# Kernel tuning notes

Measured on AMD Instinct MI355X. Metric: run time of the kernel, lower is better.

## Reference

```python
import jax, jax.numpy as jnp
import numpy as np
from jax import lax

REGION_SIZE = 5      # local window side (init kwarg)
BANDWIDTH = 0.1      # KDE kernel bandwidth (init kwarg)
NUM_BINS = 256       # intensity histogram bins
EPS = 1e-10


def setup_inputs() -> dict:
    key = jax.random.key(0)
    # image-like inputs in [0, 255] to match the 256 intensity bins
    x = jax.random.uniform(key, (8, 3, 96, 96), dtype=jnp.float32) * 255.0
    return {"x": x}


def reference(x):
    # x: [B, C, H, W]
    bins = jnp.arange(NUM_BINS, dtype=x.dtype)            # [256]
    # derivative-of-sigmoid KDE kernel evaluated at each (pixel, bin) pair
    d = (x[..., None] - bins) / BANDWIDTH                 # [B,C,H,W,256]
    sig = jax.nn.sigmoid(d)
    k = sig * (1.0 - sig)                                 # [B,C,H,W,256]
    # accumulate kernel mass over the region_size x region_size window
    # (stride 1, centered -> SAME padding), per bin
    p = lax.reduce_window(
        k, jnp.float32(0.0), lax.add,
        window_dimensions=(1, 1, REGION_SIZE, REGION_SIZE, 1),
        window_strides=(1, 1, 1, 1, 1),
        padding='SAME')                                   # [B,C,H,W,256]
    # normalize to a probability distribution over bins
    p = p / (jnp.sum(p, axis=-1, keepdims=True) + EPS)
    # Shannon entropy per pixel
    return -jnp.sum(p * jnp.log(p + EPS), axis=-1)        # [B,C,H,W]
```

## Files before the change

### kernel.cpp

```cpp
#include <hip/hip_runtime.h>
#include <hip/hip_fp16.h>
#include <stdint.h>


#define W   96
#define H   96
#define WP  100
#define IMG (W*H)
#define IMGP (WP*WP)
#define TPB 256

#if __has_builtin(__builtin_amdgcn_logf)
__device__ __forceinline__ float rawlog2(float v) {
    return __builtin_amdgcn_logf(v);
}
#else
__device__ __forceinline__ float rawlog2(float v) {
    float r;
    asm("v_log_f32 %0, %1\n\ts_nop 1" : "=v"(r) : "v"(v));
    return r;
}
#endif

__global__ __launch_bounds__(TPB) void mass_kernel(
    const float* __restrict__ x, uint4* __restrict__ wm, int total2)
{
    const int pid = blockIdx.x * TPB + threadIdx.x;
    if (pid >= total2) return;
    const int x2  = pid % WP;
    const int y2  = (pid / WP) % WP;
    const int img = pid / IMGP;

    uint4 e;
    if (x2 >= 2 && x2 < WP - 2 && y2 >= 2 && y2 < WP - 2) {
        const float v  = x[img * IMG + (y2 - 2) * W + (x2 - 2)];
        const int   b0 = (int)v;
        const float f  = v - (float)b0;
        const float E  = __expf(-10.f * f);
        const float E2 = __expf(10.f * f - 10.f);
        const float r0 = __builtin_amdgcn_rcpf(1.f + E);
        const float r1 = __builtin_amdgcn_rcpf(1.f + E2);
        const float k0 = E  * r0 * r0;
        const float k1 = E2 * r1 * r1;
        const __half2 hk = __floats2half2_rn(k0, k1);
        const float2  kc = __half22float2(hk);
        e.x = __builtin_bit_cast(uint32_t, hk);
        e.y = (uint32_t)(b0 << 4);
        e.z = __builtin_bit_cast(uint32_t, kc.x);
        e.w = __builtin_bit_cast(uint32_t, kc.y);
    } else {
        e.x = 0u;
        e.y = (uint32_t)(1 << 20);
        e.z = 0u;
        e.w = 0u;
    }
    wm[pid] = e;
}

__global__ __launch_bounds__(TPB) void entropy_kde_kernel(
    const uint4* __restrict__ wm, float* __restrict__ out)
{
    const int px   = blockIdx.x * TPB + threadIdx.x;
    const int xcol = px % W;
    const int y    = (px / W) % H;
    const int img  = px / IMG;
    const uint4* __restrict__ wb = wm + img * IMGP + y * WP + xcol;

    uint64_t pk64[25];
    int      bsh [25];
    float S0 = 0.f, S1 = 0.f;
    float T0 = 0.f, T1 = 0.f, T2a = 0.f, T3 = 0.f;

    #pragma unroll
    for (int i = 0; i < 25; ++i) {
        const int dy = i / 5, dx = i % 5;
        const uint4 m = wb[dy * WP + dx];
        const int   A  = (int)m.y + 32;
        const float k0 = __builtin_bit_cast(float, m.z);
        const float k1 = __builtin_bit_cast(float, m.w);
        if (i & 1) S1 += k0 + k1; else S0 += k0 + k1;

        uint32_t Ppk = 0u;
        #pragma unroll
        for (int j = 0; j < i; ++j) {
            int s = A - bsh[j];
            s = s < 0 ? 0 : (s > 63 ? 63 : s);
            const uint32_t t = (uint32_t)(pk64[j] >> s);
            const __half2 sum = __hadd2(__builtin_bit_cast(__half2, Ppk),
                                        __builtin_bit_cast(__half2, t));
            Ppk = __builtin_bit_cast(uint32_t, sum);
        }
        const float2 P  = __half22float2(__builtin_bit_cast(__half2, Ppk));
        const float z0 = P.x + k0, z1 = P.y + k1;
        const float t4 = z0  * rawlog2(z0  + 1e-10f) - P.x * rawlog2(P.x + 1e-10f)
                       + z1  * rawlog2(z1  + 1e-10f) - P.y * rawlog2(P.y + 1e-10f);
        if      ((i & 3) == 0) T0  += t4;
        else if ((i & 3) == 1) T1  += t4;
        else if ((i & 3) == 2) T2a += t4;
        else                   T3  += t4;

        bsh[i]  = (int)m.y;
        pk64[i] = ((uint64_t)m.x) << 32;
    }

    const float S  = (S0 + S1) + 1e-10f;
    const float T  = (T0 + T1) + (T2a + T3);
    out[px] = 0.69314718056f * (rawlog2(S) - T / S);
}

extern "C" void kernel_launch(void* const* d_in, const int* in_sizes, int n_in,
                              void* d_out, int out_size, void* d_ws, size_t ws_size,
                              hipStream_t stream)
{
    const float* x = (const float*)d_in[0];
    float* out = (float*)d_out;
    uint4* wm  = (uint4*)d_ws;
    const int total  = in_sizes[0];
    const int total2 = (total / IMG) * IMGP;
    mass_kernel<<<(total2 + TPB - 1) / TPB, TPB, 0, stream>>>(x, wm, total2);
    entropy_kde_kernel<<<total / TPB, TPB, 0, stream>>>(wm, out);
}
```

Measured before the change: 70.24 us.

## Shrink intermediate record to uint2 and reorder pairwise loop to outer-source form

The per-pixel intermediate record drops from 16 to 8 bytes: the float copies of the two kernel values are removed and reconstructed from the packed half2 in the entropy kernel. The pairwise accumulation loop is restructured so each earlier window element j is broadcast-shifted into all later accumulators P[i], with all 25 loads issued up front. The aim is to halve workspace traffic and shorten the serial dependency chain per accumulator. In exchange, 25 live half2 accumulators add register pressure, and the S sums now use the half-rounded values.

```diff
diff --git a/kernel.cpp b/kernel.cpp
--- a/kernel.cpp
+++ b/kernel.cpp
@@ -23,7 +23,7 @@
 #endif
 
 __global__ __launch_bounds__(TPB) void mass_kernel(
-    const float* __restrict__ x, uint4* __restrict__ wm, int total2)
+    const float* __restrict__ x, uint2* __restrict__ wm, int total2)
 {
     const int pid = blockIdx.x * TPB + threadIdx.x;
     if (pid >= total2) return;
@@ -31,7 +31,7 @@
     const int y2  = (pid / WP) % WP;
     const int img = pid / IMGP;
 
-    uint4 e;
+    uint2 e;
     if (x2 >= 2 && x2 < WP - 2 && y2 >= 2 && y2 < WP - 2) {
         const float v  = x[img * IMG + (y2 - 2) * W + (x2 - 2)];
         const int   b0 = (int)v;
@@ -43,68 +43,69 @@
         const float k0 = E  * r0 * r0;
         const float k1 = E2 * r1 * r1;
         const __half2 hk = __floats2half2_rn(k0, k1);
-        const float2  kc = __half22float2(hk);
         e.x = __builtin_bit_cast(uint32_t, hk);
         e.y = (uint32_t)(b0 << 4);
-        e.z = __builtin_bit_cast(uint32_t, kc.x);
-        e.w = __builtin_bit_cast(uint32_t, kc.y);
     } else {
         e.x = 0u;
         e.y = (uint32_t)(1 << 20);
-        e.z = 0u;
-        e.w = 0u;
     }
     wm[pid] = e;
 }
 
 __global__ __launch_bounds__(TPB) void entropy_kde_kernel(
-    const uint4* __restrict__ wm, float* __restrict__ out)
+    const uint2* __restrict__ wm, float* __restrict__ out)
 {
     const int px   = blockIdx.x * TPB + threadIdx.x;
     const int xcol = px % W;
     const int y    = (px / W) % H;
     const int img  = px / IMG;
-    const uint4* __restrict__ wb = wm + img * IMGP + y * WP + xcol;
+    const uint2* __restrict__ wb = wm + img * IMGP + y * WP + xcol;
 
-    uint64_t pk64[25];
-    int      bsh [25];
-    float S0 = 0.f, S1 = 0.f;
-    float T0 = 0.f, T1 = 0.f, T2a = 0.f, T3 = 0.f;
+    uint32_t pk [25];
+    int      bsh[25];
+    uint32_t P  [25];
 
     #pragma unroll
     for (int i = 0; i < 25; ++i) {
-        const int dy = i / 5, dx = i % 5;
-        const uint4 m = wb[dy * WP + dx];
-        const int   A  = (int)m.y + 32;
-        const float k0 = __builtin_bit_cast(float, m.z);
-        const float k1 = __builtin_bit_cast(float, m.w);
-        if (i & 1) S1 += k0 + k1; else S0 += k0 + k1;
+        const uint2 m = wb[(i / 5) * WP + (i % 5)];
+        pk[i]  = m.x;
+        bsh[i] = (int)m.y;
+        P[i]   = 0u;
+    }
 
-        uint32_t Ppk = 0u;
+    #pragma unroll
+    for (int j = 0; j < 24; ++j) {
+        const uint64_t pkj = ((uint64_t)pk[j]) << 32;
+        const int      cj  = 32 - bsh[j];
         #pragma unroll
-        for (int j = 0; j < i; ++j) {
-            int s = A - bsh[j];
+        for (int i = j + 1; i < 25; ++i) {
+            int s = bsh[i] + cj;
             s = s < 0 ? 0 : (s > 63 ? 63 : s);
-            const uint32_t t = (uint32_t)(pk64[j] >> s);
-            const __half2 sum = __hadd2(__builtin_bit_cast(__half2, Ppk),
+            const uint32_t t = (uint32_t)(pkj >> s);
+            const __half2 sum = __hadd2(__builtin_bit_cast(__half2, P[i]),
                                         __builtin_bit_cast(__half2, t));
-            Ppk = __builtin_bit_cast(uint32_t, sum);
+            P[i] = __builtin_bit_cast(uint32_t, sum);
         }
-        const float2 P  = __half22float2(__builtin_bit_cast(__half2, Ppk));
-        const float z0 = P.x + k0, z1 = P.y + k1;
-        const float t4 = z0  * rawlog2(z0  + 1e-10f) - P.x * rawlog2(P.x + 1e-10f)
-                       + z1  * rawlog2(z1  + 1e-10f) - P.y * rawlog2(P.y + 1e-10f);
+    }
+
+    float S0 = 0.f, S1 = 0.f;
+    float T0 = 0.f, T1 = 0.f, T2a = 0.f, T3 = 0.f;
+    #pragma unroll
+    for (int i = 0; i < 25; ++i) {
+        const float2 kc = __half22float2(__builtin_bit_cast(__half2, pk[i]));
+        const float2 Pv = __half22float2(__builtin_bit_cast(__half2, P[i]));
+        if (i & 1) S1 += kc.x + kc.y; else S0 += kc.x + kc.y;
+        const float z0 = Pv.x + kc.x, z1 = Pv.y + kc.y;
+        const float t4 = z0 * rawlog2(z0 + 1e-10f) - Pv.x * rawlog2(Pv.x + 1e-10f)
+                       + z1 * rawlog2(z1 + 1e-10f) - Pv.y * rawlog2(Pv.y + 1e-10f);
         if      ((i & 3) == 0) T0  += t4;
         else if ((i & 3) == 1) T1  += t4;
         else if ((i & 3) == 2) T2a += t4;
         else                   T3  += t4;
-
-        bsh[i]  = (int)m.y;
-        pk64[i] = ((uint64_t)m.x) << 32;
     }
 
-    const float S  = (S0 + S1) + 1e-10f;
-    const float T  = (T0 + T1) + (T2a + T3);
+    const float S = (S0 + S1) + 1e-10f;
+    const float T = (T0 + T1) + (T2a + T3);
     out[px] = 0.69314718056f * (rawlog2(S) - T / S);
 }
 
@@ -114,7 +115,7 @@
 {
     const float* x = (const float*)d_in[0];
     float* out = (float*)d_out;
-    uint4* wm  = (uint4*)d_ws;
+    uint2* wm  = (uint2*)d_ws;
     const int total  = in_sizes[0];
     const int total2 = (total / IMG) * IMGP;
     mass_kernel<<<(total2 + TPB - 1) / TPB, TPB, 0, stream>>>(x, wm, total2);
```

Result: no change. 70.26 us (+0.0%).
